# Performance work log

Measured on AMD Instinct MI355X. Metric: run time of the kernel, lower is better.

The kernel has to match this reference:

```python
import jax, jax.numpy as jnp
import numpy as np

B, S, P, N, V = 8, 16, 32, 2048, 2562
K_SAMPLE = 500      # samples_per_slot
K_NEAREST = 3
MIN_DIST = 0.5
FALLOFF = 5.0
GW, SW, RW = 0.7, 0.3, 0.2


def _icosphere(level=4):
    t = (1.0 + 5.0 ** 0.5) / 2.0
    v = np.array([[-1, t, 0], [1, t, 0], [-1, -t, 0], [1, -t, 0],
                  [0, -1, t], [0, 1, t], [0, -1, -t], [0, 1, -t],
                  [t, 0, -1], [t, 0, 1], [-t, 0, -1], [-t, 0, 1]], dtype=np.float64)
    v /= np.linalg.norm(v, axis=1, keepdims=True)
    f = [[0, 11, 5], [0, 5, 1], [0, 1, 7], [0, 7, 10], [0, 10, 11],
         [1, 5, 9], [5, 11, 4], [11, 10, 2], [10, 7, 6], [7, 1, 8],
         [3, 9, 4], [3, 4, 2], [3, 2, 6], [3, 6, 8], [3, 8, 9],
         [4, 9, 5], [2, 4, 11], [6, 2, 10], [8, 6, 7], [9, 8, 1]]
    verts = [x for x in v]
    for _ in range(level):
        cache = {}
        def mid(a, b):
            key = (min(a, b), max(a, b))
            if key in cache:
                return cache[key]
            m = verts[a] + verts[b]
            m = m / np.linalg.norm(m)
            verts.append(m)
            cache[key] = len(verts) - 1
            return cache[key]
        nf = []
        for a, b, c in f:
            ab, bc, ca = mid(a, b), mid(b, c), mid(c, a)
            nf += [[a, ab, ca], [b, bc, ab], [c, ca, bc], [ab, bc, ca]]
        f = nf
    return np.asarray(verts, dtype=np.float32)


def _euler_xyz_to_matrix(ang):
    # pytorch3d euler_angles_to_matrix(..., 'XYZ'): R = Rx(a) @ Ry(b) @ Rz(c)
    a, b, c = ang[..., 0], ang[..., 1], ang[..., 2]
    ca, sa = jnp.cos(a), jnp.sin(a)
    cb, sb = jnp.cos(b), jnp.sin(b)
    cc, sc = jnp.cos(c), jnp.sin(c)
    o, z = jnp.ones_like(a), jnp.zeros_like(a)
    sh = ang.shape[:-1] + (3, 3)
    Rx = jnp.stack([o, z, z, z, ca, -sa, z, sa, ca], -1).reshape(sh)
    Ry = jnp.stack([cb, z, sb, z, o, z, -sb, z, cb], -1).reshape(sh)
    Rz = jnp.stack([cc, -sc, z, sc, cc, z, z, z, o], -1).reshape(sh)
    return Rx @ Ry @ Rz


def _cdist2(x, y):
    # squared euclidean distances: x [..., n, 3], y [..., m, 3] -> [..., n, m]
    x2 = (x * x).sum(-1)[..., :, None]
    y2 = (y * y).sum(-1)[..., None, :]
    return jnp.maximum(x2 + y2 - 2.0 * jnp.einsum('...nd,...md->...nm', x, y), 0.0)


def _forward(scales, transforms, prototype_weights, prototype_offsets, target_pcl, verts):
    # --- transform_mesh ---
    R = _euler_xyz_to_matrix(transforms[..., 3:])          # [B,S,P,3,3]
    deformed = verts[None] + prototype_offsets              # [P,V,3]
    rotated = jnp.einsum('pvj,bspij->bspvi', deformed, R)   # verts @ R^T
    scaled = rotated * scales[:, :, None, None, :]          # [B,S,P,V,3]
    translated = scaled + transforms[:, :, :, None, :3]
    final = jnp.einsum('bspvi,bsp->bsvi', translated, prototype_weights)  # [B,S,V,3]

    # --- hybrid chamfer loss ---
    pred = final[:, :, :K_SAMPLE, :]                        # deterministic per-slot samples
    pred_flat = pred.reshape(B, S * K_SAMPLE, 3)
    # global: target -> all predicted points, mean of K nearest squared dists
    d2g = _cdist2(target_pcl, pred_flat)                    # [B,N,S*K]
    knn = -jax.lax.top_k(-d2g, K_NEAREST)[0]
    global_loss = knn.mean()
    # per-slot: each slot's points -> target, nearest neighbor squared dist
    d2s = _cdist2(pred, target_pcl[:, None])                # [B,S,K,N]
    per_slot_loss = d2s.min(-1).mean()
    # centroid repulsion
    cent = final.mean(axis=2)                               # [B,S,3]
    eye = jnp.eye(S, dtype=final.dtype)
    d = jnp.sqrt(_cdist2(cent, cent) + eye)                 # eye keeps diag grads finite
    rep = jnp.exp(FALLOFF * jnp.maximum(MIN_DIST - d, 0.0)) * (1.0 - eye)
    rep_loss = (rep.sum(axis=(1, 2)) / (S * (S - 1))).mean()

    return GW * global_loss + SW * per_slot_loss + RW * rep_loss


def setup_inputs() -> dict:
    key = jax.random.key(0)
    ks = jax.random.split(key, 5)
    scales = jax.random.uniform(ks[0], (B, S, 1), jnp.float32) * 0.5 + 0.5
    transforms = jax.random.normal(ks[1], (B, S, P, 6), jnp.float32)
    w = jax.random.uniform(ks[2], (B, S, P), jnp.float32) + 1e-3
    prototype_weights = w / w.sum(-1, keepdims=True)
    prototype_offsets = jax.random.normal(ks[3], (P, V, 3), jnp.float32) * 0.1
    target_pcl = jax.random.normal(ks[4], (B, N, 3), jnp.float32)
    verts = jnp.asarray(_icosphere(4))                      # [2562,3]
    return {"scales": scales, "transforms": transforms,
            "prototype_weights": prototype_weights,
            "prototype_offsets": prototype_offsets,
            "target_pcl": target_pcl, "verts": verts}


def reference(scales, transforms, prototype_weights, prototype_offsets, target_pcl, verts):
    return _forward(scales, transforms, prototype_weights, prototype_offsets, target_pcl, verts)
```

## Files before the change

### kernel.cpp

```cpp
#include <hip/hip_runtime.h>
#include <math.h>

namespace {
constexpr int cB = 8, cS = 16, cP = 32, cN = 2048, cV = 2562;
constexpr int cK = 500;
constexpr int cJ = cS * cK;
constexpr int cJC = 16;
constexpr int cJCH = cJ / cJC;
constexpr int cNC = 8;
constexpr int cNCH = cN / cNC;
constexpr int cJPAD = 8192;
constexpr float FINF = 3.402823466e+38f;

constexpr int OFF_PRED4 = 0;
constexpr int OFF_TGT4  = OFF_PRED4 + cB * cJ * 4;
constexpr int OFF_CENT  = OFF_TGT4 + cB * cN * 4;
constexpr int OFF_VBAR  = OFF_CENT + cB * cS * 3;
constexpr int OFF_OBAR  = OFF_VBAR + 4;
constexpr int OFF_T3    = 322048;
constexpr int OFF_PSP   = OFF_T3 + cB * cN * cJC * 3;
constexpr int OFF_GM    = OFF_PSP + cB * cNC * cJPAD;
constexpr int OFF_PS    = OFF_GM + 64;
}

__device__ __forceinline__ float block_sum(float v, float* red, int tid) {
  red[tid] = v;
  __syncthreads();
  for (int s = 128; s > 0; s >>= 1) {
    if (tid < s) red[tid] += red[tid + s];
    __syncthreads();
  }
  return red[0];
}

__global__ void k_prep(const float* __restrict__ verts,
                       const float* __restrict__ offs,
                       const float* __restrict__ target,
                       float* __restrict__ ws) {
  const int blk = blockIdx.x;
  const int tid = threadIdx.x;
  if (blk <= cP) {
    __shared__ float red[256];
    const float* src = (blk < cP) ? (offs + blk * cV * 3) : verts;
    float acc0 = 0.f, acc1 = 0.f, acc2 = 0.f;
    for (int v = tid; v < cV; v += 256) {
      acc0 += src[v * 3 + 0];
      acc1 += src[v * 3 + 1];
      acc2 += src[v * 3 + 2];
    }
    float* dst = (blk < cP) ? (ws + OFF_OBAR + blk * 3) : (ws + OFF_VBAR);
    float a[3] = {acc0, acc1, acc2};
    for (int c = 0; c < 3; ++c) {
      float s = block_sum(a[c], red, tid);
      if (tid == 0) dst[c] = s / (float)cV;
      __syncthreads();
    }
  } else {
    const int idx = (blk - (cP + 1)) * 256 + tid;
    const float x = target[idx * 3 + 0];
    const float y = target[idx * 3 + 1];
    const float z = target[idx * 3 + 2];
    float4* o = (float4*)(ws + OFF_TGT4);
    o[idx] = make_float4(x, y, z, 0.5f * fmaf(x, x, fmaf(y, y, z * z)));
  }
}

__global__ void k_pred(const float* __restrict__ scales,
                       const float* __restrict__ transforms,
                       const float* __restrict__ pw,
                       const float* __restrict__ offs,
                       const float* __restrict__ verts,
                       float* __restrict__ ws) {
  const int bs = blockIdx.x;
  const int tid = threadIdx.x;
  __shared__ float sM[cP][9];
  __shared__ float sWT[cP][3];
  __shared__ float sC[3];
  if (tid < cP) {
    const int p = tid;
    const float* t = transforms + (bs * cP + p) * 6;
    const float w = pw[bs * cP + p];
    const float sc = scales[bs];
    const float a = t[3], b = t[4], c = t[5];
    const float ca = cosf(a), sa = sinf(a);
    const float cb = cosf(b), sb = sinf(b);
    const float cg = cosf(c), sg = sinf(c);
    const float f = w * sc;
    sM[p][0] = f * (cb * cg);
    sM[p][1] = f * (-cb * sg);
    sM[p][2] = f * (sb);
    sM[p][3] = f * (ca * sg + sa * sb * cg);
    sM[p][4] = f * (ca * cg - sa * sb * sg);
    sM[p][5] = f * (-sa * cb);
    sM[p][6] = f * (sa * sg - ca * sb * cg);
    sM[p][7] = f * (sa * cg + ca * sb * sg);
    sM[p][8] = f * (ca * cb);
    sWT[p][0] = w * t[0];
    sWT[p][1] = w * t[1];
    sWT[p][2] = w * t[2];
  }
  __syncthreads();
  if (tid < 3) {
    float s = 0.f;
    for (int p = 0; p < cP; ++p) s += sWT[p][tid];
    sC[tid] = s;
  }
  __syncthreads();
  for (int k = tid; k < cK; k += blockDim.x) {
    const float x0 = verts[k * 3 + 0], x1 = verts[k * 3 + 1], x2 = verts[k * 3 + 2];
    float a0 = sC[0], a1 = sC[1], a2 = sC[2];
#pragma unroll 8
    for (int p = 0; p < cP; ++p) {
      const float* o = offs + (p * cV + k) * 3;
      const float d0 = x0 + o[0], d1 = x1 + o[1], d2 = x2 + o[2];
      a0 = fmaf(sM[p][0], d0, fmaf(sM[p][1], d1, fmaf(sM[p][2], d2, a0)));
      a1 = fmaf(sM[p][3], d0, fmaf(sM[p][4], d1, fmaf(sM[p][5], d2, a1)));
      a2 = fmaf(sM[p][6], d0, fmaf(sM[p][7], d1, fmaf(sM[p][8], d2, a2)));
    }
    float4* pr = (float4*)(ws + OFF_PRED4);
    pr[bs * cK + k] =
        make_float4(a0, a1, a2, 0.5f * fmaf(a0, a0, fmaf(a1, a1, a2 * a2)));
  }
  if (tid == 0) {
    const float* vb = ws + OFF_VBAR;
    float c0 = sC[0], c1 = sC[1], c2 = sC[2];
    for (int p = 0; p < cP; ++p) {
      const float* ob = ws + OFF_OBAR + p * 3;
      const float d0 = vb[0] + ob[0], d1 = vb[1] + ob[1], d2 = vb[2] + ob[2];
      c0 += sM[p][0] * d0 + sM[p][1] * d1 + sM[p][2] * d2;
      c1 += sM[p][3] * d0 + sM[p][4] * d1 + sM[p][5] * d2;
      c2 += sM[p][6] * d0 + sM[p][7] * d1 + sM[p][8] * d2;
    }
    float* ct = ws + OFF_CENT + bs * 3;
    ct[0] = c0; ct[1] = c1; ct[2] = c2;
  }
}

__global__ void __launch_bounds__(256) k_global(float* __restrict__ ws) {
  __shared__ float4 sP[cJCH];
  const int nb = blockIdx.x, jc = blockIdx.y, b = blockIdx.z;
  const int tid = threadIdx.x;
  const float4* pr = (const float4*)(ws + OFF_PRED4) + b * cJ + jc * cJCH;
  for (int i = tid; i < cJCH; i += 256) sP[i] = pr[i];
  __syncthreads();
  const int n = nb * 256 + tid;
  const float4* tg = (const float4*)(ws + OFF_TGT4) + b * cN;
  const float4 tA = tg[n];
  const float4 tB = tg[n + 1024];
  float a0 = FINF, a1 = FINF, a2 = FINF;
  float b0 = FINF, b1 = FINF, b2 = FINF;
  for (int j = 0; j < cJCH; ++j) {
    const float4 p = sP[j];
    const float sA = fmaf(-tA.x, p.x, fmaf(-tA.y, p.y, fmaf(-tA.z, p.z, p.w)));
    const float sB = fmaf(-tB.x, p.x, fmaf(-tB.y, p.y, fmaf(-tB.z, p.z, p.w)));
    float h;
    h = fmaxf(a0, sA); a0 = fminf(a0, sA);
    { const float h1 = fmaxf(a1, h); a1 = fminf(a1, h); a2 = fminf(a2, h1); }
    h = fmaxf(b0, sB); b0 = fminf(b0, sB);
    { const float h1 = fmaxf(b1, h); b1 = fminf(b1, h); b2 = fminf(b2, h1); }
  }
  float* oA = ws + OFF_T3 + ((b * cN + n) * cJC + jc) * 3;
  oA[0] = a0; oA[1] = a1; oA[2] = a2;
  float* oB = ws + OFF_T3 + ((b * cN + n + 1024) * cJC + jc) * 3;
  oB[0] = b0; oB[1] = b1; oB[2] = b2;
}

__global__ void k_gmerge(float* __restrict__ ws) {
  __shared__ float red[256];
  const int tid = threadIdx.x;
  const int idx = blockIdx.x * 256 + tid;
  const float* tp = ws + OFF_T3 + idx * cJC * 3;
  float t0 = FINF, t1 = FINF, t2 = FINF;
#pragma unroll
  for (int q = 0; q < cJC * 3; ++q) {
    const float d = tp[q];
    const float h0 = fmaxf(t0, d); t0 = fminf(t0, d);
    const float h1 = fmaxf(t1, h0); t1 = fminf(t1, h0);
    t2 = fminf(t2, h1);
  }
  const float ht = ws[OFF_TGT4 + idx * 4 + 3];
  const float d0 = fmaxf(2.f * (t0 + ht), 0.f);
  const float d1 = fmaxf(2.f * (t1 + ht), 0.f);
  const float d2 = fmaxf(2.f * (t2 + ht), 0.f);
  const float s = block_sum(d0 + d1 + d2, red, tid);
  if (tid == 0) ws[OFF_GM + blockIdx.x] = s;
}

__global__ void __launch_bounds__(256) k_perslot(float* __restrict__ ws) {
  __shared__ float4 sT[cNCH];
  const int jb = blockIdx.x;
  const int nc = blockIdx.y;
  const int b = blockIdx.z;
  const int tid = threadIdx.x;
  const float4* tg = (const float4*)(ws + OFF_TGT4) + b * cN + nc * cNCH;
  sT[tid] = tg[tid];
  __syncthreads();
  const float4* pr = (const float4*)(ws + OFF_PRED4) + b * cJ;
  float px[4], py[4], pz[4];
  float m[4] = {FINF, FINF, FINF, FINF};
#pragma unroll
  for (int q = 0; q < 4; ++q) {
    int j = jb * 1024 + q * 256 + tid;
    j = (j < cJ) ? j : (cJ - 1);
    const float4 p = pr[j];
    px[q] = p.x; py[q] = p.y; pz[q] = p.z;
  }
  for (int n = 0; n < cNCH; ++n) {
    const float4 t = sT[n];
#pragma unroll
    for (int q = 0; q < 4; ++q) {
      const float s = fmaf(-px[q], t.x, fmaf(-py[q], t.y, fmaf(-pz[q], t.z, t.w)));
      m[q] = fminf(m[q], s);
    }
  }
  float* o = ws + OFF_PSP + (b * cNC + nc) * cJPAD + jb * 1024 + tid;
#pragma unroll
  for (int q = 0; q < 4; ++q) o[q * 256] = m[q];
}

__global__ void k_psmerge(float* __restrict__ ws) {
  __shared__ float red[256];
  const int tid = threadIdx.x;
  const int b = blockIdx.y;
  const int j = blockIdx.x * 256 + tid;
  float contrib = 0.f;
  if (j < cJ) {
    float m = FINF;
#pragma unroll
    for (int nc = 0; nc < cNC; ++nc)
      m = fminf(m, ws[OFF_PSP + (b * cNC + nc) * cJPAD + j]);
    const float hp = ws[OFF_PRED4 + (b * cJ + j) * 4 + 3];
    contrib = fmaxf(2.f * (m + hp), 0.f);
  }
  const float s = block_sum(contrib, red, tid);
  if (tid == 0) ws[OFF_PS + b * 32 + blockIdx.x] = s;
}

__global__ void k_final(float* __restrict__ ws, float* __restrict__ out) {
  __shared__ float red[256];
  const int tid = threadIdx.x;
  const float* cent = ws + OFF_CENT;
  float acc = 0.f;
  for (int idx = tid; idx < cB * cS * cS; idx += 256) {
    const int b = idx / (cS * cS);
    const int r = idx % (cS * cS);
    const int i = r / cS, jj = r % cS;
    if (i == jj) continue;
    const float* ci = cent + (b * cS + i) * 3;
    const float* cj = cent + (b * cS + jj) * 3;
    const float dx = ci[0] - cj[0], dy = ci[1] - cj[1], dz = ci[2] - cj[2];
    const float d = sqrtf(fmaf(dx, dx, fmaf(dy, dy, dz * dz)));
    acc += expf(5.0f * fmaxf(0.5f - d, 0.0f));
  }
  const float repsum = block_sum(acc, red, tid);
  __syncthreads();
  const float gsum = block_sum((tid < 64) ? ws[OFF_GM + tid] : 0.f, red, tid);
  __syncthreads();
  const float pssum = block_sum(ws[OFF_PS + tid], red, tid);
  if (tid == 0) {
    const float global_loss = gsum / (float)(cB * cN * 3);
    const float per_slot = pssum / (float)(cB * cS * cK);
    const float rep = repsum / (float)(cB * cS * (cS - 1));
    out[0] = 0.7f * global_loss + 0.3f * per_slot + 0.2f * rep;
  }
}

extern "C" void kernel_launch(void* const* d_in, const int* in_sizes, int n_in,
                              void* d_out, int out_size, void* d_ws, size_t ws_size,
                              hipStream_t stream) {
  const float* scales     = (const float*)d_in[0];
  const float* transforms = (const float*)d_in[1];
  const float* pw         = (const float*)d_in[2];
  const float* offs       = (const float*)d_in[3];
  const float* target     = (const float*)d_in[4];
  const float* verts      = (const float*)d_in[5];
  float* out = (float*)d_out;
  float* ws = (float*)d_ws;

  k_prep<<<cP + 1 + (cB * cN) / 256, 256, 0, stream>>>(verts, offs, target, ws);
  k_pred<<<cB * cS, 256, 0, stream>>>(scales, transforms, pw, offs, verts, ws);
  k_global<<<dim3(cN / 512, cJC, cB), 256, 0, stream>>>(ws);
  k_perslot<<<dim3(cJPAD / 1024, cNC, cB), 256, 0, stream>>>(ws);
  k_gmerge<<<(cB * cN) / 256, 256, 0, stream>>>(ws);
  k_psmerge<<<dim3(cJPAD / 256, cB), 256, 0, stream>>>(ws);
  k_final<<<1, 256, 0, stream>>>(ws, out);
}
```

Before: 76.46 us.

## Fuse prep/pred and merge kernels, use med3 top-3 and planar partial layout

Merges the prep and prediction kernels into one launch by moving the slot-centroid calculation into the final kernel, which reads the per-slot matrices saved to workspace. The two merge kernels become one launch. The global top-3 partials move to a plane-major layout so the merge reads them coalesced, and the top-3 insertion uses fmed3. Unroll pragmas are added to the inner loops. This cuts launch count and serialization but makes the single-block final kernel do more work.

```diff
diff --git a/kernel.cpp b/kernel.cpp
--- a/kernel.cpp
+++ b/kernel.cpp
@@ -10,17 +10,19 @@
 constexpr int cNC = 8;
 constexpr int cNCH = cN / cNC;
 constexpr int cJPAD = 8192;
+constexpr int cBN = cB * cN;
 constexpr float FINF = 3.402823466e+38f;
 
 constexpr int OFF_PRED4 = 0;
-constexpr int OFF_TGT4  = OFF_PRED4 + cB * cJ * 4;
-constexpr int OFF_CENT  = OFF_TGT4 + cB * cN * 4;
-constexpr int OFF_VBAR  = OFF_CENT + cB * cS * 3;
-constexpr int OFF_OBAR  = OFF_VBAR + 4;
-constexpr int OFF_T3    = 322048;
-constexpr int OFF_PSP   = OFF_T3 + cB * cN * cJC * 3;
-constexpr int OFF_GM    = OFF_PSP + cB * cNC * cJPAD;
-constexpr int OFF_PS    = OFF_GM + 64;
+constexpr int OFF_TGT4  = 256000;
+constexpr int OFF_VBAR  = 321536;
+constexpr int OFF_OBAR  = 321540;
+constexpr int OFF_SM    = 321664;
+constexpr int OFF_SC    = 358528;
+constexpr int OFF_T3    = 358912;
+constexpr int OFF_PSP   = 1145344;
+constexpr int OFF_GM    = 1669632;
+constexpr int OFF_PS    = 1669696;
 }
 
 __device__ __forceinline__ float block_sum(float v, float* red, int tid) {
@@ -33,10 +35,21 @@
   return red[0];
 }
 
-__global__ void k_prep(const float* __restrict__ verts,
-                       const float* __restrict__ offs,
-                       const float* __restrict__ target,
-                       float* __restrict__ ws) {
+__device__ __forceinline__ void top3_insert(float& t0, float& t1, float& t2, float d) {
+  const float nt2 = fminf(t2, fmaxf(t1, d));
+  const float nt1 = __builtin_amdgcn_fmed3f(t0, t1, d);
+  t0 = fminf(t0, d);
+  t1 = nt1;
+  t2 = nt2;
+}
+
+__global__ void __launch_bounds__(256) k_front(const float* __restrict__ scales,
+                                               const float* __restrict__ transforms,
+                                               const float* __restrict__ pw,
+                                               const float* __restrict__ offs,
+                                               const float* __restrict__ verts,
+                                               const float* __restrict__ target,
+                                               float* __restrict__ ws) {
   const int blk = blockIdx.x;
   const int tid = threadIdx.x;
   if (blk <= cP) {
@@ -55,84 +68,64 @@
       if (tid == 0) dst[c] = s / (float)cV;
       __syncthreads();
     }
-  } else {
+  } else if (blk <= cP + 64) {
     const int idx = (blk - (cP + 1)) * 256 + tid;
     const float x = target[idx * 3 + 0];
     const float y = target[idx * 3 + 1];
     const float z = target[idx * 3 + 2];
-    float4* o = (float4*)(ws + OFF_TGT4);
-    o[idx] = make_float4(x, y, z, 0.5f * fmaf(x, x, fmaf(y, y, z * z)));
-  }
-}
-
-__global__ void k_pred(const float* __restrict__ scales,
-                       const float* __restrict__ transforms,
-                       const float* __restrict__ pw,
-                       const float* __restrict__ offs,
-                       const float* __restrict__ verts,
-                       float* __restrict__ ws) {
-  const int bs = blockIdx.x;
-  const int tid = threadIdx.x;
-  __shared__ float sM[cP][9];
-  __shared__ float sWT[cP][3];
-  __shared__ float sC[3];
-  if (tid < cP) {
-    const int p = tid;
-    const float* t = transforms + (bs * cP + p) * 6;
-    const float w = pw[bs * cP + p];
-    const float sc = scales[bs];
-    const float a = t[3], b = t[4], c = t[5];
-    const float ca = cosf(a), sa = sinf(a);
-    const float cb = cosf(b), sb = sinf(b);
-    const float cg = cosf(c), sg = sinf(c);
-    const float f = w * sc;
-    sM[p][0] = f * (cb * cg);
-    sM[p][1] = f * (-cb * sg);
-    sM[p][2] = f * (sb);
-    sM[p][3] = f * (ca * sg + sa * sb * cg);
-    sM[p][4] = f * (ca * cg - sa * sb * sg);
-    sM[p][5] = f * (-sa * cb);
-    sM[p][6] = f * (sa * sg - ca * sb * cg);
-    sM[p][7] = f * (sa * cg + ca * sb * sg);
-    sM[p][8] = f * (ca * cb);
-    sWT[p][0] = w * t[0];
-    sWT[p][1] = w * t[1];
-    sWT[p][2] = w * t[2];
-  }
-  __syncthreads();
-  if (tid < 3) {
-    float s = 0.f;
-    for (int p = 0; p < cP; ++p) s += sWT[p][tid];
-    sC[tid] = s;
-  }
-  __syncthreads();
-  for (int k = tid; k < cK; k += blockDim.x) {
-    const float x0 = verts[k * 3 + 0], x1 = verts[k * 3 + 1], x2 = verts[k * 3 + 2];
-    float a0 = sC[0], a1 = sC[1], a2 = sC[2];
+    ((float4*)(ws + OFF_TGT4))[idx] =
+        make_float4(x, y, z, 0.5f * fmaf(x, x, fmaf(y, y, z * z)));
+  } else {
+    const int bs = blk - (cP + 65);
+    __shared__ float sM[cP][9];
+    __shared__ float sC[3];
+    __shared__ float sWT[cP][3];
+    if (tid < cP) {
+      const int p = tid;
+      const float* t = transforms + (bs * cP + p) * 6;
+      const float w = pw[bs * cP + p];
+      const float sc = scales[bs];
+      const float a = t[3], b = t[4], c = t[5];
+      const float ca = cosf(a), sa = sinf(a);
+      const float cb = cosf(b), sb = sinf(b);
+      const float cg = cosf(c), sg = sinf(c);
+      const float f = w * sc;
+      sM[p][0] = f * (cb * cg);
+      sM[p][1] = f * (-cb * sg);
+      sM[p][2] = f * (sb);
+      sM[p][3] = f * (ca * sg + sa * sb * cg);
+      sM[p][4] = f * (ca * cg - sa * sb * sg);
+      sM[p][5] = f * (-sa * cb);
+      sM[p][6] = f * (sa * sg - ca * sb * cg);
+      sM[p][7] = f * (sa * cg + ca * sb * sg);
+      sM[p][8] = f * (ca * cb);
+      sWT[p][0] = w * t[0];
+      sWT[p][1] = w * t[1];
+      sWT[p][2] = w * t[2];
+    }
+    __syncthreads();
+    if (tid < 3) {
+      float s = 0.f;
+      for (int p = 0; p < cP; ++p) s += sWT[p][tid];
+      sC[tid] = s;
+    }
+    __syncthreads();
+    if (tid < cP * 9) ws[OFF_SM + bs * 288 + tid] = ((const float*)sM)[tid];
+    if (tid < 3) ws[OFF_SC + bs * 3 + tid] = sC[tid];
+    for (int k = tid; k < cK; k += 256) {
+      const float x0 = verts[k * 3 + 0], x1 = verts[k * 3 + 1], x2 = verts[k * 3 + 2];
+      float a0 = sC[0], a1 = sC[1], a2 = sC[2];
 #pragma unroll 8
-    for (int p = 0; p < cP; ++p) {
-      const float* o = offs + (p * cV + k) * 3;
-      const float d0 = x0 + o[0], d1 = x1 + o[1], d2 = x2 + o[2];
-      a0 = fmaf(sM[p][0], d0, fmaf(sM[p][1], d1, fmaf(sM[p][2], d2, a0)));
-      a1 = fmaf(sM[p][3], d0, fmaf(sM[p][4], d1, fmaf(sM[p][5], d2, a1)));
-      a2 = fmaf(sM[p][6], d0, fmaf(sM[p][7], d1, fmaf(sM[p][8], d2, a2)));
-    }
-    float4* pr = (float4*)(ws + OFF_PRED4);
-    pr[bs * cK + k] =
-        make_float4(a0, a1, a2, 0.5f * fmaf(a0, a0, fmaf(a1, a1, a2 * a2)));
-  }
-  if (tid == 0) {
-    const float* vb = ws + OFF_VBAR;
-    float c0 = sC[0], c1 = sC[1], c2 = sC[2];
-    for (int p = 0; p < cP; ++p) {
-      const float* ob = ws + OFF_OBAR + p * 3;
-      const float d0 = vb[0] + ob[0], d1 = vb[1] + ob[1], d2 = vb[2] + ob[2];
-      c0 += sM[p][0] * d0 + sM[p][1] * d1 + sM[p][2] * d2;
-      c1 += sM[p][3] * d0 + sM[p][4] * d1 + sM[p][5] * d2;
-      c2 += sM[p][6] * d0 + sM[p][7] * d1 + sM[p][8] * d2;
-    }
-    float* ct = ws + OFF_CENT + bs * 3;
-    ct[0] = c0; ct[1] = c1; ct[2] = c2;
+      for (int p = 0; p < cP; ++p) {
+        const float* o = offs + (p * cV + k) * 3;
+        const float d0 = x0 + o[0], d1 = x1 + o[1], d2 = x2 + o[2];
+        a0 = fmaf(sM[p][0], d0, fmaf(sM[p][1], d1, fmaf(sM[p][2], d2, a0)));
+        a1 = fmaf(sM[p][3], d0, fmaf(sM[p][4], d1, fmaf(sM[p][5], d2, a1)));
+        a2 = fmaf(sM[p][6], d0, fmaf(sM[p][7], d1, fmaf(sM[p][8], d2, a2)));
+      }
+      ((float4*)(ws + OFF_PRED4))[bs * cK + k] =
+          make_float4(a0, a1, a2, 0.5f * fmaf(a0, a0, fmaf(a1, a1, a2 * a2)));
+    }
   }
 }
 
@@ -149,41 +142,22 @@
   const float4 tB = tg[n + 1024];
   float a0 = FINF, a1 = FINF, a2 = FINF;
   float b0 = FINF, b1 = FINF, b2 = FINF;
+#pragma unroll 4
   for (int j = 0; j < cJCH; ++j) {
     const float4 p = sP[j];
     const float sA = fmaf(-tA.x, p.x, fmaf(-tA.y, p.y, fmaf(-tA.z, p.z, p.w)));
     const float sB = fmaf(-tB.x, p.x, fmaf(-tB.y, p.y, fmaf(-tB.z, p.z, p.w)));
-    float h;
-    h = fmaxf(a0, sA); a0 = fminf(a0, sA);
-    { const float h1 = fmaxf(a1, h); a1 = fminf(a1, h); a2 = fminf(a2, h1); }
-    h = fmaxf(b0, sB); b0 = fminf(b0, sB);
-    { const float h1 = fmaxf(b1, h); b1 = fminf(b1, h); b2 = fminf(b2, h1); }
-  }
-  float* oA = ws + OFF_T3 + ((b * cN + n) * cJC + jc) * 3;
-  oA[0] = a0; oA[1] = a1; oA[2] = a2;
-  float* oB = ws + OFF_T3 + ((b * cN + n + 1024) * cJC + jc) * 3;
-  oB[0] = b0; oB[1] = b1; oB[2] = b2;
-}
-
-__global__ void k_gmerge(float* __restrict__ ws) {
-  __shared__ float red[256];
-  const int tid = threadIdx.x;
-  const int idx = blockIdx.x * 256 + tid;
-  const float* tp = ws + OFF_T3 + idx * cJC * 3;
-  float t0 = FINF, t1 = FINF, t2 = FINF;
-#pragma unroll
-  for (int q = 0; q < cJC * 3; ++q) {
-    const float d = tp[q];
-    const float h0 = fmaxf(t0, d); t0 = fminf(t0, d);
-    const float h1 = fmaxf(t1, h0); t1 = fminf(t1, h0);
-    t2 = fminf(t2, h1);
-  }
-  const float ht = ws[OFF_TGT4 + idx * 4 + 3];
-  const float d0 = fmaxf(2.f * (t0 + ht), 0.f);
-  const float d1 = fmaxf(2.f * (t1 + ht), 0.f);
-  const float d2 = fmaxf(2.f * (t2 + ht), 0.f);
-  const float s = block_sum(d0 + d1 + d2, red, tid);
-  if (tid == 0) ws[OFF_GM + blockIdx.x] = s;
+    top3_insert(a0, a1, a2, sA);
+    top3_insert(b0, b1, b2, sB);
+  }
+  float* plane = ws + OFF_T3 + (jc * 3) * cBN;
+  const int idxA = b * cN + n;
+  plane[0 * cBN + idxA] = a0;
+  plane[1 * cBN + idxA] = a1;
+  plane[2 * cBN + idxA] = a2;
+  plane[0 * cBN + idxA + 1024] = b0;
+  plane[1 * cBN + idxA + 1024] = b1;
+  plane[2 * cBN + idxA + 1024] = b2;
 }
 
 __global__ void __launch_bounds__(256) k_perslot(float* __restrict__ ws) {
@@ -205,6 +179,7 @@
     const float4 p = pr[j];
     px[q] = p.x; py[q] = p.y; pz[q] = p.z;
   }
+#pragma unroll 2
   for (int n = 0; n < cNCH; ++n) {
     const float4 t = sT[n];
 #pragma unroll
@@ -218,36 +193,74 @@
   for (int q = 0; q < 4; ++q) o[q * 256] = m[q];
 }
 
-__global__ void k_psmerge(float* __restrict__ ws) {
+__global__ void __launch_bounds__(256) k_merge(float* __restrict__ ws) {
   __shared__ float red[256];
-  const int tid = threadIdx.x;
-  const int b = blockIdx.y;
-  const int j = blockIdx.x * 256 + tid;
-  float contrib = 0.f;
-  if (j < cJ) {
-    float m = FINF;
-#pragma unroll
-    for (int nc = 0; nc < cNC; ++nc)
-      m = fminf(m, ws[OFF_PSP + (b * cNC + nc) * cJPAD + j]);
-    const float hp = ws[OFF_PRED4 + (b * cJ + j) * 4 + 3];
-    contrib = fmaxf(2.f * (m + hp), 0.f);
-  }
-  const float s = block_sum(contrib, red, tid);
-  if (tid == 0) ws[OFF_PS + b * 32 + blockIdx.x] = s;
-}
-
-__global__ void k_final(float* __restrict__ ws, float* __restrict__ out) {
+  const int blk = blockIdx.x;
+  const int tid = threadIdx.x;
+  if (blk < 64) {
+    const int idx = blk * 256 + tid;
+    const float* plane = ws + OFF_T3;
+    float t0 = FINF, t1 = FINF, t2 = FINF;
+#pragma unroll
+    for (int q = 0; q < cJC * 3; ++q)
+      top3_insert(t0, t1, t2, plane[q * cBN + idx]);
+    const float ht = ws[OFF_TGT4 + idx * 4 + 3];
+    const float d0 = fmaxf(2.f * (t0 + ht), 0.f);
+    const float d1 = fmaxf(2.f * (t1 + ht), 0.f);
+    const float d2 = fmaxf(2.f * (t2 + ht), 0.f);
+    const float s = block_sum(d0 + d1 + d2, red, tid);
+    if (tid == 0) ws[OFF_GM + blk] = s;
+  } else {
+    const int rb = blk - 64;
+    const int b = rb >> 5;
+    const int jb = rb & 31;
+    const int j = jb * 256 + tid;
+    float contrib = 0.f;
+    if (j < cJ) {
+      float m = FINF;
+#pragma unroll
+      for (int nc = 0; nc < cNC; ++nc)
+        m = fminf(m, ws[OFF_PSP + (b * cNC + nc) * cJPAD + j]);
+      const float hp = ws[OFF_PRED4 + (b * cJ + j) * 4 + 3];
+      contrib = fmaxf(2.f * (m + hp), 0.f);
+    }
+    const float s = block_sum(contrib, red, tid);
+    if (tid == 0) ws[OFF_PS + b * 32 + jb] = s;
+  }
+}
+
+__global__ void __launch_bounds__(256) k_final(float* __restrict__ ws, float* __restrict__ out) {
   __shared__ float red[256];
-  const int tid = threadIdx.x;
-  const float* cent = ws + OFF_CENT;
+  __shared__ float scent[cB * cS * 3];
+  const int tid = threadIdx.x;
+  if (tid < cB * cS) {
+    const int bs = tid;
+    const float* M = ws + OFF_SM + bs * 288;
+    const float* vb = ws + OFF_VBAR;
+    float c0 = ws[OFF_SC + bs * 3 + 0];
+    float c1 = ws[OFF_SC + bs * 3 + 1];
+    float c2 = ws[OFF_SC + bs * 3 + 2];
+#pragma unroll 8
+    for (int p = 0; p < cP; ++p) {
+      const float* ob = ws + OFF_OBAR + p * 3;
+      const float d0 = vb[0] + ob[0], d1 = vb[1] + ob[1], d2 = vb[2] + ob[2];
+      c0 = fmaf(M[p * 9 + 0], d0, fmaf(M[p * 9 + 1], d1, fmaf(M[p * 9 + 2], d2, c0)));
+      c1 = fmaf(M[p * 9 + 3], d0, fmaf(M[p * 9 + 4], d1, fmaf(M[p * 9 + 5], d2, c1)));
+      c2 = fmaf(M[p * 9 + 6], d0, fmaf(M[p * 9 + 7], d1, fmaf(M[p * 9 + 8], d2, c2)));
+    }
+    scent[bs * 3 + 0] = c0;
+    scent[bs * 3 + 1] = c1;
+    scent[bs * 3 + 2] = c2;
+  }
+  __syncthreads();
   float acc = 0.f;
   for (int idx = tid; idx < cB * cS * cS; idx += 256) {
     const int b = idx / (cS * cS);
     const int r = idx % (cS * cS);
     const int i = r / cS, jj = r % cS;
     if (i == jj) continue;
-    const float* ci = cent + (b * cS + i) * 3;
-    const float* cj = cent + (b * cS + jj) * 3;
+    const float* ci = scent + (b * cS + i) * 3;
+    const float* cj = scent + (b * cS + jj) * 3;
     const float dx = ci[0] - cj[0], dy = ci[1] - cj[1], dz = ci[2] - cj[2];
     const float d = sqrtf(fmaf(dx, dx, fmaf(dy, dy, dz * dz)));
     acc += expf(5.0f * fmaxf(0.5f - d, 0.0f));
@@ -277,11 +290,10 @@
   float* out = (float*)d_out;
   float* ws = (float*)d_ws;
 
-  k_prep<<<cP + 1 + (cB * cN) / 256, 256, 0, stream>>>(verts, offs, target, ws);
-  k_pred<<<cB * cS, 256, 0, stream>>>(scales, transforms, pw, offs, verts, ws);
+  k_front<<<cP + 1 + 64 + cB * cS, 256, 0, stream>>>(scales, transforms, pw, offs,
+                                                     verts, target, ws);
   k_global<<<dim3(cN / 512, cJC, cB), 256, 0, stream>>>(ws);
   k_perslot<<<dim3(cJPAD / 1024, cNC, cB), 256, 0, stream>>>(ws);
-  k_gmerge<<<(cB * cN) / 256, 256, 0, stream>>>(ws);
-  k_psmerge<<<dim3(cJPAD / 256, cB), 256, 0, stream>>>(ws);
+  k_merge<<<64 + 256, 256, 0, stream>>>(ws);
   k_final<<<1, 256, 0, stream>>>(ws, out);
 }
```

Result: faster. 68.30 us (-10.7%).
